# Kernel tuning notes

Measured on AMD Instinct MI355X. Metric: run time of the kernel, lower is better.

## Reference

```python
import jax, jax.numpy as jnp
import numpy as np

D_MODEL = 128; D_STATE = 16; D_CONV = 4; EXPAND = 2
D_INNER = EXPAND * D_MODEL          # 256
DT_RANK = (D_MODEL + 15) // 16      # 8 (ceil(d_model/16), Mamba default)
B, NF, H, W = 4, 32, 16, 16         # L = NF*H*W = 8192 tokens


def _layer_norm(x, w, b, eps=1e-5):
    m = x.mean(-1, keepdims=True)
    v = ((x - m) ** 2).mean(-1, keepdims=True)
    return (x - m) * jax.lax.rsqrt(v + eps) * w + b


def _causal_conv(x, w, b):
    # x: [B, L, D_INNER]; w: [D_INNER, 1, D_CONV] depthwise causal conv along L
    y = jax.lax.conv_general_dilated(
        jnp.swapaxes(x, 1, 2), w, (1,), [(D_CONV - 1, 0)],
        dimension_numbers=('NCH', 'OIH', 'NCH'), feature_group_count=D_INNER)
    return jnp.swapaxes(y + b[None, :, None], 1, 2)


def _mamba_dir(xi, z, conv_w, conv_b, xproj_w, dtproj_w, dtproj_b, A_log, Dskip):
    # One direction of the bidirectional Mamba block (selective scan).
    xc = jax.nn.silu(_causal_conv(xi, conv_w, conv_b))            # [B,L,Di]
    dbl = xc @ xproj_w.T                                          # [B,L,dt_rank+2n]
    dt_r, Bm, Cm = jnp.split(dbl, [DT_RANK, DT_RANK + D_STATE], axis=-1)
    dt = jax.nn.softplus(dt_r @ dtproj_w.T + dtproj_b)            # [B,L,Di]
    A = -jnp.exp(A_log)                                           # [Di,n]

    def step(h, inp):
        dt_t, B_t, C_t, x_t = inp                                 # [B,Di],[B,n],[B,n],[B,Di]
        h = jnp.exp(dt_t[:, :, None] * A) * h + (dt_t * x_t)[:, :, None] * B_t[:, None, :]
        return h, jnp.einsum('bdn,bn->bd', h, C_t)

    h0 = jnp.zeros((xi.shape[0], D_INNER, D_STATE), xi.dtype)
    xs = tuple(jnp.swapaxes(a, 0, 1) for a in (dt, Bm, Cm, xc))   # L-leading
    _, ys = jax.lax.scan(step, h0, xs)                            # [L,B,Di]
    y = jnp.swapaxes(ys, 0, 1) + xc * Dskip
    return y * jax.nn.silu(z)


def setup_inputs() -> dict:
    key = jax.random.key(0)
    ks = jax.random.split(key, 12)
    wrand = lambda k, shape: jax.random.normal(k, shape, jnp.float32) * 0.02
    # S4D-real init: A = [1..d_state] per channel
    A_init = jnp.log(jnp.tile(jnp.arange(1, D_STATE + 1, dtype=jnp.float32)[None, :], (D_INNER, 1)))
    dt_bias = jnp.full((D_INNER,), -4.6, jnp.float32)  # softplus^-1(~0.01)
    return {
        'x': jax.random.normal(ks[0], (B, D_MODEL, NF, H, W), jnp.float32),
        'ln1_w': jnp.ones((D_MODEL,), jnp.float32), 'ln1_b': jnp.zeros((D_MODEL,), jnp.float32),
        'ln2_w': jnp.ones((D_MODEL,), jnp.float32), 'ln2_b': jnp.zeros((D_MODEL,), jnp.float32),
        'in_proj_w': wrand(ks[1], (2 * D_INNER, D_MODEL)),
        'out_proj_w': wrand(ks[2], (D_MODEL, D_INNER)),
        'conv_w_f': wrand(ks[3], (D_INNER, 1, D_CONV)), 'conv_b_f': jnp.zeros((D_INNER,), jnp.float32),
        'xproj_w_f': wrand(ks[4], (DT_RANK + 2 * D_STATE, D_INNER)),
        'dtproj_w_f': wrand(ks[5], (D_INNER, DT_RANK)), 'dtproj_b_f': dt_bias,
        'A_log_f': A_init, 'D_f': jnp.ones((D_INNER,), jnp.float32),
        'conv_w_b': wrand(ks[6], (D_INNER, 1, D_CONV)), 'conv_b_b': jnp.zeros((D_INNER,), jnp.float32),
        'xproj_w_b': wrand(ks[7], (DT_RANK + 2 * D_STATE, D_INNER)),
        'dtproj_w_b': wrand(ks[8], (D_INNER, DT_RANK)), 'dtproj_b_b': dt_bias,
        'A_log_b': A_init, 'D_b': jnp.ones((D_INNER,), jnp.float32),
    }


def reference(x, ln1_w, ln1_b, ln2_w, ln2_b, in_proj_w, out_proj_w,
              conv_w_f, conv_b_f, xproj_w_f, dtproj_w_f, dtproj_b_f, A_log_f, D_f,
              conv_w_b, conv_b_b, xproj_w_b, dtproj_w_b, dtproj_b_b, A_log_b, D_b):
    b, d, nf, h, w = x.shape
    L = nf * h * w
    x_flat = jnp.swapaxes(x.reshape(b, d, L), 1, 2)               # [B,L,d_model]
    xn = _layer_norm(x_flat, ln1_w, ln1_b)
    xz = xn @ in_proj_w.T                                          # [B,L,2*Di]
    xi, z = jnp.split(xz, 2, axis=-1)
    y_f = _mamba_dir(xi, z, conv_w_f, conv_b_f, xproj_w_f, dtproj_w_f, dtproj_b_f, A_log_f, D_f)
    y_b = _mamba_dir(xi[:, ::-1], z[:, ::-1], conv_w_b, conv_b_b, xproj_w_b,
                     dtproj_w_b, dtproj_b_b, A_log_b, D_b)[:, ::-1]
    out = (y_f + y_b) @ out_proj_w.T                               # shared out_proj
    x_out = _layer_norm(x_flat + out, ln2_w, ln2_b)                # residual + norm2
    return jnp.swapaxes(x_out, 1, 2).reshape(b, d, nf, h, w)
```

## Files before the change

kernel.cpp:

```cpp
#include <hip/hip_runtime.h>

#define NB   4
#define LSEQ 8192
#define DM   128
#define DI   256
#define NS   16
#define RK   8
#define NCH  256
#define LC   32
#define MTOT (NB*LSEQ)
#define LOG2E 1.44269504088896340736f
#define LN2f  0.69314718055994530942f

#if __has_builtin(__builtin_amdgcn_exp2f)
__device__ __forceinline__ float fexp2(float x){ return __builtin_amdgcn_exp2f(x); }
#else
__device__ __forceinline__ float fexp2(float x){ return exp2f(x); }
#endif
#if __has_builtin(__builtin_amdgcn_logf)
__device__ __forceinline__ float flog2(float x){ return __builtin_amdgcn_logf(x); }
#else
__device__ __forceinline__ float flog2(float x){ return log2f(x); }
#endif
#if __has_builtin(__builtin_amdgcn_rcpf)
__device__ __forceinline__ float frcp(float x){ return __builtin_amdgcn_rcpf(x); }
#else
__device__ __forceinline__ float frcp(float x){ return 1.f/x; }
#endif
__device__ __forceinline__ float fexpn(float x){ return fexp2(x*LOG2E); }
__device__ __forceinline__ float fsilu(float x){ return x*frcp(1.f + fexpn(-x)); }
__device__ __forceinline__ float fsoftplus(float x){
  return fmaxf(x,0.f) + flog2(1.f + fexpn(-fabsf(x)))*LN2f;
}

__device__ __forceinline__ unsigned short f2bf(float v){
  unsigned int u = __float_as_uint(v);
  return (unsigned short)((u + 0x7FFFu + ((u >> 16) & 1u)) >> 16);
}
__device__ __forceinline__ float bf2f(unsigned short h){
  return __uint_as_float(((unsigned int)h) << 16);
}

typedef __attribute__((ext_vector_type(8))) short bf16x8;
typedef __attribute__((ext_vector_type(4))) float f32x4;
typedef __attribute__((ext_vector_type(2))) float f32x2;

#if __has_builtin(__builtin_elementwise_fma)
__device__ __forceinline__ f32x2 pkfma(f32x2 a, f32x2 b, f32x2 c){ return __builtin_elementwise_fma(a,b,c); }
#else
__device__ __forceinline__ f32x2 pkfma(f32x2 a, f32x2 b, f32x2 c){ return a*b + c; }
#endif

__global__ __launch_bounds__(256) void k_prep_w(
    const float* __restrict__ wip, unsigned short* __restrict__ wipbf,
    const float* __restrict__ xwf, const float* __restrict__ xwb, unsigned short* __restrict__ xwbf,
    const float* __restrict__ wop, unsigned short* __restrict__ wopbf)
{
  int i = blockIdx.x*256 + threadIdx.x;
  if (i < 65536) {
    wipbf[i] = f2bf(wip[i]);
  } else if (i < 90112) {
    int j = i - 65536;
    int dirw = j / 12288;
    int rem = j - dirw*12288;
    int row = rem >> 8, k = rem & 255;
    const float* src = dirw ? xwb : xwf;
    xwbf[j] = (row < 40) ? f2bf(src[row*256 + k]) : (unsigned short)0;
  } else {
    int j = i - 90112;
    wopbf[j] = f2bf(wop[j]);
  }
}

__global__ __launch_bounds__(256) void k_ln(
    const float* __restrict__ x, const float* __restrict__ ln1w, const float* __restrict__ ln1b,
    unsigned short* __restrict__ xnbf)
{
  __shared__ float a_s[DM][65];
  __shared__ float mS[64], rS[64];
  const int tid = threadIdx.x;
  const int m0 = blockIdx.x * 64;
  const int b = m0 >> 13, l0 = m0 & (LSEQ-1);
  const float* xb = x + b*DM*LSEQ;
#pragma unroll
  for (int i = 0; i < 32; ++i) {
    int idx = tid + i*256;
    int d = idx >> 6, l = idx & 63;
    a_s[d][l] = xb[d*LSEQ + l0 + l];
  }
  __syncthreads();
  {
    int p = tid & 3, l = tid >> 2;
    float s = 0.f, q = 0.f;
#pragma unroll
    for (int jj = 0; jj < 32; ++jj) {
      float v = a_s[p + 4*jj][l];
      s += v; q += v*v;
    }
    s += __shfl_xor(s,1); s += __shfl_xor(s,2);
    q += __shfl_xor(q,1); q += __shfl_xor(q,2);
    float m = s*(1.f/DM);
    float var = q*(1.f/DM) - m*m;
    if (p == 0) { mS[l] = m; rS[l] = rsqrtf(var + 1e-5f); }
  }
  __syncthreads();
#pragma unroll
  for (int i = 0; i < 32; ++i) {
    int idx = tid + i*256;
    int l = idx >> 7, d = idx & 127;
    float v = (a_s[d][l] - mS[l])*rS[l]*ln1w[d] + ln1b[d];
    xnbf[(m0+l)*DM + d] = f2bf(v);
  }
}

__global__ __launch_bounds__(256) void k_gemm_in(
    const unsigned short* __restrict__ xnbf, const unsigned short* __restrict__ wipbf,
    unsigned short* __restrict__ xib, unsigned short* __restrict__ zzb)
{
  __shared__ char lds[32768];
  const int tid = threadIdx.x;
  const int m0 = blockIdx.x * 64;
  const int n0 = blockIdx.y * 64;
  const unsigned short* srcs[2] = { xnbf + m0*DM, wipbf + n0*DM };
#pragma unroll
  for (int p = 0; p < 2; ++p) {
#pragma unroll
    for (int i = 0; i < 4; ++i) {
      int u = tid + i*256;
      int row = u >> 4, c = u & 15;
      int dstu = p*1024 + row*16 + (c ^ (row & 7));
      *(uint4*)(lds + dstu*16) = *(const uint4*)(srcs[p] + row*DM + c*8);
    }
  }
  __syncthreads();
  const int wid = tid >> 6, lane = tid & 63;
  const int m0w = (wid & 1)*32, n0w = (wid >> 1)*32;
  const int lr = lane & 15, kg = lane >> 4;
  bf16x8 af[2][4], bfv[2][4];
#pragma unroll
  for (int mi = 0; mi < 2; ++mi) {
    int row = m0w + mi*16 + lr;
#pragma unroll
    for (int kk = 0; kk < 4; ++kk) {
      int slot = (kk*4 + kg) ^ (row & 7);
      af[mi][kk] = *(const bf16x8*)(lds + row*256 + slot*16);
    }
  }
#pragma unroll
  for (int nj = 0; nj < 2; ++nj) {
    int row = n0w + nj*16 + lr;
#pragma unroll
    for (int kk = 0; kk < 4; ++kk) {
      int slot = (kk*4 + kg) ^ (row & 7);
      bfv[nj][kk] = *(const bf16x8*)(lds + 16384 + row*256 + slot*16);
    }
  }
  f32x4 acc[2][2];
#pragma unroll
  for (int mi = 0; mi < 2; ++mi)
#pragma unroll
    for (int nj = 0; nj < 2; ++nj) acc[mi][nj] = 0.f;
#pragma unroll
  for (int kk = 0; kk < 4; ++kk)
#pragma unroll
    for (int mi = 0; mi < 2; ++mi)
#pragma unroll
      for (int nj = 0; nj < 2; ++nj)
        acc[mi][nj] = __builtin_amdgcn_mfma_f32_16x16x32_bf16(af[mi][kk], bfv[nj][kk], acc[mi][nj], 0,0,0);
  if (n0 < 256) {
#pragma unroll
    for (int mi = 0; mi < 2; ++mi)
#pragma unroll
      for (int nj = 0; nj < 2; ++nj) {
        int n_g = n0 + n0w + nj*16 + lr;
#pragma unroll
        for (int r = 0; r < 4; ++r) {
          int m_g = m0 + m0w + mi*16 + kg*4 + r;
          xib[(size_t)m_g*DI + n_g] = f2bf(acc[mi][nj][r]);
        }
      }
  } else {
#pragma unroll
    for (int mi = 0; mi < 2; ++mi)
#pragma unroll
      for (int nj = 0; nj < 2; ++nj) {
        int n_g = (n0 - 256) + n0w + nj*16 + lr;
#pragma unroll
        for (int r = 0; r < 4; ++r) {
          int m_g = m0 + m0w + mi*16 + kg*4 + r;
          zzb[(size_t)m_g*DI + n_g] = f2bf(fsilu(acc[mi][nj][r]));
        }
      }
  }
}

__global__ __launch_bounds__(256) void k_conv_xproj(
  const unsigned short* __restrict__ xib,
  const float* __restrict__ cwf, const float* __restrict__ cbf,
  const float* __restrict__ cwb, const float* __restrict__ cbb,
  const unsigned short* __restrict__ xwbf,
  const float* __restrict__ dtwf, const float* __restrict__ dtbf,
  const float* __restrict__ dtwb, const float* __restrict__ dtbb,
  float* __restrict__ Bm, float* __restrict__ Cm,
  unsigned int* __restrict__ xdt)
{
  __shared__ char lds[57344];
  __shared__ float dtr_s[64][8];
  const int tid = threadIdx.x, bid = blockIdx.x;
  const int lt = bid & (LSEQ/64 - 1);
  const int b  = (bid >> 7) & 3;
  const int dir = bid >> 9;
  const int l0 = lt*64;
  const int db = dir*NB + b;
  const unsigned short* xwp = xwbf + dir*48*256;
#pragma unroll
  for (int i = 0; i < 6; ++i) {
    int u = tid + i*256;
    int row = u >> 5, s = u & 31;
    *(uint4*)(lds + 32768 + row*512 + ((s ^ (row & 7))<<4)) =
        *(const uint4*)(xwp + row*256 + s*8);
  }
  const float* cw  = dir ? cwb : cwf;
  const float* cbp = dir ? cbb : cbf;
  const int d = tid;
  const float w0 = cw[d*4+0], w1 = cw[d*4+1], w2 = cw[d*4+2], w3 = cw[d*4+3];
  const float bias = cbp[d];
  const int g0 = dir ? (LSEQ-1-l0) : l0;
  const int stp = dir ? -DI : DI;
  const unsigned short* xp = xib + (size_t)(b*LSEQ)*DI + d + (size_t)g0*DI;
  float h3 = 0.f, h2 = 0.f, h1 = 0.f;
  if (l0 >= 3) { h3 = bf2f(xp[-3*stp]); h2 = bf2f(xp[-2*stp]); h1 = bf2f(xp[-1*stp]); }
  float r0 = bf2f(xp[0]), r1 = bf2f(xp[stp]), r2 = bf2f(xp[2*stp]), r3 = bf2f(xp[3*stp]);
  for (int j = 0; j < 64; j += 4) {
    float v0 = r0, v1 = r1, v2 = r2, v3 = r3;
    if (j + 4 < 64) {
      const unsigned short* q = xp + (j+4)*stp;
      r0 = bf2f(q[0]); r1 = bf2f(q[stp]); r2 = bf2f(q[2*stp]); r3 = bf2f(q[3*stp]);
    }
#pragma unroll
    for (int u = 0; u < 4; ++u) {
      float vv = (u==0)?v0:(u==1)?v1:(u==2)?v2:v3;
      float a = bias + w0*h3 + w1*h2 + w2*h1 + w3*vv;
      int row = j + u;
      *(unsigned short*)(lds + row*512 + ((((d>>3) ^ (row&7))<<4) + ((d&7)<<1))) = f2bf(fsilu(a));
      h3 = h2; h2 = h1; h1 = vv;
    }
  }
  __syncthreads();
  const int wid = tid >> 6, lane = tid & 63;
  const int lr = lane & 15, kg = lane >> 4;
  const int arow = wid*16 + lr;
  f32x4 acc[3];
#pragma unroll
  for (int j = 0; j < 3; ++j) acc[j] = 0.f;
#pragma unroll
  for (int t = 0; t < 8; ++t) {
    bf16x8 afv = *(const bf16x8*)(lds + arow*512 + (((t*4+kg) ^ (arow&7))<<4));
#pragma unroll
    for (int j = 0; j < 3; ++j) {
      int wrow = j*16 + lr;
      bf16x8 bfr = *(const bf16x8*)(lds + 32768 + wrow*512 + (((t*4+kg) ^ (wrow&7))<<4));
      acc[j] = __builtin_amdgcn_mfma_f32_16x16x32_bf16(afv, bfr, acc[j], 0,0,0);
    }
  }
  const int base_l = (db*LSEQ + l0) + wid*16 + kg*4;
  const int rloc = wid*16 + kg*4;
#pragma unroll
  for (int j = 0; j < 3; ++j) {
    int col = j*16 + lr;
#pragma unroll
    for (int r = 0; r < 4; ++r) {
      float v = acc[j][r];
      if (col < 8)       dtr_s[rloc + r][col] = v;
      else if (col < 24) Bm[(size_t)(base_l + r)*NS + col - 8] = v;
      else if (col < 40) Cm[(size_t)(base_l + r)*NS + col - 24] = v;
    }
  }
  __syncthreads();
  const float* dtw = dir ? dtwb : dtwf;
  const float* dtbp= dir ? dtbb : dtbf;
  float dwv[8];
  *(float4*)(dwv+0) = *(const float4*)&dtw[d*RK];
  *(float4*)(dwv+4) = *(const float4*)&dtw[d*RK+4];
  const float dtbv = dtbp[d];
  unsigned int* xdtp = xdt + (size_t)(db*LSEQ + l0)*DI + d;
  for (int row = 0; row < 64; ++row) {
    float sd = dtbv;
#pragma unroll
    for (int r = 0; r < RK; ++r) sd = fmaf(dtr_s[row][r], dwv[r], sd);
    unsigned short dtb = f2bf(fsoftplus(sd));
    unsigned short xcb = *(const unsigned short*)(lds + row*512 + ((((d>>3) ^ (row&7))<<4) + ((d&7)<<1)));
    xdtp[(size_t)row*DI] = (unsigned int)xcb | ((unsigned int)dtb << 16);
  }
}

__global__ __launch_bounds__(256) void k_scan_local(
  const unsigned int* __restrict__ xdt, const float* __restrict__ Bm,
  const float* __restrict__ alogf, const float* __restrict__ alogb,
  unsigned short* __restrict__ hloc, float* __restrict__ sumdt)
{
  __shared__ float Bc[LC][NS];
  const int tid = threadIdx.x, bid = blockIdx.x;
  const int c = bid & (NCH-1), b = (bid>>8)&3, dir = bid>>10;
  const int db = dir*NB + b;
  const int l0 = c*LC;
  for (int i = tid; i < LC*NS; i += 256) (&Bc[0][0])[i] = Bm[(size_t)(db*LSEQ + l0)*NS + i];
  const float* alog = dir ? alogb : alogf;
  const int d = tid;
  float A2[NS];
#pragma unroll
  for (int n = 0; n < NS; ++n) A2[n] = -fexpn(alog[d*NS+n]) * LOG2E;
  const float a20 = A2[0];
  bool pw = true;
#pragma unroll
  for (int n = 1; n < NS; ++n) pw = pw && (fabsf(A2[n] - (n+1)*a20) <= 1e-3f*fabsf(A2[n]));
  f32x2 h2[8];
#pragma unroll
  for (int k = 0; k < 8; ++k) h2[k] = 0.f;
  const unsigned int* xp = xdt + (size_t)(db*LSEQ + l0)*DI + d;
  unsigned int u0 = xp[0], u1 = xp[DI], u2 = xp[2*DI], u3 = xp[3*DI];
  __syncthreads();
  float sac = 0.f;
  for (int j = 0; j < LC; j += 4) {
    unsigned int w0=u0, w1=u1, w2=u2, w3=u3;
    if (j + 4 < LC) {
      const unsigned int* q = xp + (size_t)(j+4)*DI;
      u0=q[0]; u1=q[DI]; u2=q[2*DI]; u3=q[3*DI];
    }
#pragma unroll
    for (int u = 0; u < 4; ++u) {
      unsigned int uu = (u==0)?w0:(u==1)?w1:(u==2)?w2:w3;
      float xc = __uint_as_float(uu << 16);
      float dt = __uint_as_float(uu & 0xffff0000u);
      sac += dt;
      float dx = dt*xc;
      f32x2 e2[8];
      if (pw) {
        float e1 = fexp2(a20*dt);
        float es = e1*e1;
        f32x2 esq = {es, es};
        e2[0] = (f32x2){e1, es};
#pragma unroll
        for (int k = 1; k < 8; ++k) e2[k] = e2[k-1]*esq;
      } else {
#pragma unroll
        for (int k = 0; k < 8; ++k)
          e2[k] = (f32x2){fexp2(A2[2*k]*dt), fexp2(A2[2*k+1]*dt)};
      }
      const f32x2* bb2 = (const f32x2*)&Bc[j+u][0];
      f32x2 dx2 = {dx, dx};
#pragma unroll
      for (int k = 0; k < 8; ++k) h2[k] = pkfma(h2[k], e2[k], bb2[k]*dx2);
    }
  }
  unsigned int hp8[8];
#pragma unroll
  for (int k = 0; k < 8; ++k)
    hp8[k] = (unsigned int)f2bf(h2[k].x) | ((unsigned int)f2bf(h2[k].y) << 16);
  unsigned short* dst = hloc + ((size_t)(db*NCH + c)*DI + d)*NS;
  *(uint4*)(dst)   = *(uint4*)(hp8);
  *(uint4*)(dst+8) = *(uint4*)(hp8+4);
  sumdt[(size_t)(db*NCH + c)*DI + d] = sac;
}

__global__ __launch_bounds__(64) void k_prefix(
  unsigned short* __restrict__ hloc, const float* __restrict__ sumdt,
  const float* __restrict__ alogf, const float* __restrict__ alogb)
{
  const int gid = blockIdx.x*64 + threadIdx.x;
  const int n = gid & 15;
  const int d = (gid >> 4) & 255;
  const int db = gid >> 12;
  const float* alog = (db >= NB) ? alogb : alogf;
  const float a2 = -fexpn(alog[d*NS+n]) * LOG2E;
  const int HS = DI*NS;
  unsigned short* hp = hloc + (size_t)db*NCH*HS + d*NS + n;
  const float* sp = sumdt + (size_t)db*NCH*DI + d;
  float hr = 0.f;
  float bl[16], bs[16];
#pragma unroll
  for (int j = 0; j < 16; ++j) { bl[j] = bf2f(hp[(size_t)j*HS]); bs[j] = sp[(size_t)j*DI]; }
  for (int blk = 0; blk < NCH/16; ++blk) {
    float nl[16], nsv[16];
    if (blk < NCH/16 - 1) {
#pragma unroll
      for (int j = 0; j < 16; ++j) {
        nl[j]  = bf2f(hp[(size_t)(blk*16+16+j)*HS]);
        nsv[j] = sp[(size_t)(blk*16+16+j)*DI];
      }
    }
#pragma unroll
    for (int j = 0; j < 16; ++j) {
      float hl = bl[j];
      hp[(size_t)(blk*16+j)*HS] = f2bf(hr);
      hr = fmaf(fexp2(a2*bs[j]), hr, hl);
    }
    if (blk < NCH/16 - 1) {
#pragma unroll
      for (int j = 0; j < 16; ++j) { bl[j] = nl[j]; bs[j] = nsv[j]; }
    }
  }
}

__global__ __launch_bounds__(256) void k_scan_out(
  const unsigned int* __restrict__ xdt, const unsigned short* __restrict__ zzb,
  const float* __restrict__ Bm, const float* __restrict__ Cm,
  const unsigned short* __restrict__ hinb,
  const float* __restrict__ alogf, const float* __restrict__ alogb,
  const float* __restrict__ Dskf, const float* __restrict__ Dskb,
  unsigned short* __restrict__ s2bf)
{
  __shared__ float Bc[LC][NS];
  __shared__ float Cc[LC][NS];
  const int tid = threadIdx.x, bid = blockIdx.x;
  const int c = bid & (NCH-1), b = (bid>>8)&3, dir = bid>>10;
  const int db = dir*NB + b;
  const int l0 = c*LC;
  for (int i = tid; i < LC*NS; i += 256) (&Bc[0][0])[i] = Bm[(size_t)(db*LSEQ + l0)*NS + i];
  for (int i = tid; i < LC*NS; i += 256) (&Cc[0][0])[i] = Cm[(size_t)(db*LSEQ + l0)*NS + i];
  const float* alog = dir ? alogb : alogf;
  const int d = tid;
  const float Dd = (dir ? Dskb : Dskf)[d];
  float A2[NS];
#pragma unroll
  for (int n = 0; n < NS; ++n) A2[n] = -fexpn(alog[d*NS+n]) * LOG2E;
  const float a20 = A2[0];
  bool pw = true;
#pragma unroll
  for (int n = 1; n < NS; ++n) pw = pw && (fabsf(A2[n] - (n+1)*a20) <= 1e-3f*fabsf(A2[n]));
  f32x2 h2[8];
  {
    const unsigned short* hb = hinb + ((size_t)(db*NCH + c)*DI + d)*NS;
    uint4 p0 = *(const uint4*)(hb);
    uint4 p1 = *(const uint4*)(hb+8);
    unsigned int w[8] = {p0.x,p0.y,p0.z,p0.w,p1.x,p1.y,p1.z,p1.w};
#pragma unroll
    for (int k = 0; k < 8; ++k)
      h2[k] = (f32x2){__uint_as_float(w[k] << 16), __uint_as_float(w[k] & 0xffff0000u)};
  }
  const int g0 = dir ? (LSEQ-1-l0) : l0;
  const int stp = dir ? -DI : DI;
  const unsigned int* xp = xdt + (size_t)(db*LSEQ + l0)*DI + d;
  const unsigned short* zp = zzb + (size_t)(b*LSEQ + g0)*DI + d;
  unsigned short* sp = s2bf + (size_t)(db*LSEQ + l0)*DI + d;
  unsigned int u0 = xp[0], u1 = xp[DI], u2 = xp[2*DI], u3 = xp[3*DI];
  unsigned short z0 = zp[0], z1 = zp[stp], z2 = zp[2*stp], z3 = zp[3*stp];
  __syncthreads();
  for (int j = 0; j < LC; j += 4) {
    unsigned int w0=u0, w1=u1, w2=u2, w3=u3;
    unsigned short y0=z0, y1=z1, y2=z2, y3=z3;
    if (j + 4 < LC) {
      const unsigned int* q = xp + (size_t)(j+4)*DI;
      u0=q[0]; u1=q[DI]; u2=q[2*DI]; u3=q[3*DI];
      const unsigned short* qz = zp + (j+4)*stp;
      z0=qz[0]; z1=qz[stp]; z2=qz[2*stp]; z3=qz[3*stp];
    }
#pragma unroll
    for (int u = 0; u < 4; ++u) {
      unsigned int uu = (u==0)?w0:(u==1)?w1:(u==2)?w2:w3;
      unsigned short zu = (u==0)?y0:(u==1)?y1:(u==2)?y2:y3;
      float xc = __uint_as_float(uu << 16);
      float dt = __uint_as_float(uu & 0xffff0000u);
      float dx = dt*xc;
      f32x2 e2[8];
      if (pw) {
        float e1 = fexp2(a20*dt);
        float es = e1*e1;
        f32x2 esq = {es, es};
        e2[0] = (f32x2){e1, es};
#pragma unroll
        for (int k = 1; k < 8; ++k) e2[k] = e2[k-1]*esq;
      } else {
#pragma unroll
        for (int k = 0; k < 8; ++k)
          e2[k] = (f32x2){fexp2(A2[2*k]*dt), fexp2(A2[2*k+1]*dt)};
      }
      const f32x2* bb2 = (const f32x2*)&Bc[j+u][0];
      const f32x2* cc2 = (const f32x2*)&Cc[j+u][0];
      f32x2 dx2 = {dx, dx};
      f32x2 yv2 = {0.f, 0.f};
#pragma unroll
      for (int k = 0; k < 8; ++k) {
        h2[k] = pkfma(h2[k], e2[k], bb2[k]*dx2);
        yv2 = pkfma(h2[k], cc2[k], yv2);
      }
      float yv = yv2.x + yv2.y;
      yv = fmaf(xc, Dd, yv);
      sp[(size_t)(j+u)*DI] = f2bf(yv * bf2f(zu));
    }
  }
}

__global__ __launch_bounds__(512) void k_out(
  const unsigned short* __restrict__ s2bf,
  const unsigned short* __restrict__ wopbf,
  const float* __restrict__ x, const float* __restrict__ ln2w, const float* __restrict__ ln2b,
  float* __restrict__ out)
{
  __shared__ char lds[65536];
  const int tid = threadIdx.x;
  const int m0 = blockIdx.x*64;
  const int b = m0 >> 13, l0 = m0 & (LSEQ-1);
  const unsigned short* sF = s2bf + (size_t)b*LSEQ*DI;
  const unsigned short* sB = s2bf + (size_t)(NB + b)*LSEQ*DI;
#pragma unroll
  for (int i = 0; i < 8; ++i) {
    int u = tid + i*512;
    int row = u >> 6, c = u & 63;
    int l = l0 + row;
    const unsigned short* src = (c < 32) ? (sF + (size_t)l*DI + c*8)
                                         : (sB + (size_t)(LSEQ-1-l)*DI + (c-32)*8);
    *(uint4*)(lds + row*1024 + ((c ^ (row & 7))<<4)) = *(const uint4*)src;
  }
  const int wid = tid >> 6;
  const int wr = wid >> 2, wc = wid & 3;
  const int lane = tid & 63, lr = lane & 15, kg = lane >> 4;
  bf16x8 wf[2][8];
#pragma unroll
  for (int nt = 0; nt < 2; ++nt) {
    int n = wc*32 + nt*16 + lr;
#pragma unroll
    for (int kt = 0; kt < 8; ++kt)
      wf[nt][kt] = *(const bf16x8*)(wopbf + n*DI + kt*32 + kg*8);
  }
  __syncthreads();
  f32x4 acc[2][2];
#pragma unroll
  for (int mt = 0; mt < 2; ++mt)
#pragma unroll
    for (int nt = 0; nt < 2; ++nt) acc[mt][nt] = 0.f;
#pragma unroll
  for (int kt2 = 0; kt2 < 16; ++kt2) {
#pragma unroll
    for (int mt = 0; mt < 2; ++mt) {
      int row = wr*32 + mt*16 + lr;
      int slot = (kt2*4 + kg) ^ (row & 7);
      bf16x8 af = *(const bf16x8*)(lds + row*1024 + (slot<<4));
#pragma unroll
      for (int nt = 0; nt < 2; ++nt)
        acc[mt][nt] = __builtin_amdgcn_mfma_f32_16x16x32_bf16(af, wf[nt][kt2 & 7], acc[mt][nt], 0,0,0);
    }
  }
  __syncthreads();
  float* smem = (float*)lds;
  const int RP = 133;
  float* mS = smem + 64*RP;
  float* rS = mS + 64;
  const float* xb = x + b*DM*LSEQ + l0;
#pragma unroll
  for (int mt = 0; mt < 2; ++mt) {
    int mbase = wr*32 + mt*16 + kg*4;
#pragma unroll
    for (int nt = 0; nt < 2; ++nt) {
      int n = wc*32 + nt*16 + lr;
      float4 rx = *(const float4*)&xb[n*LSEQ + mbase];
      smem[(mbase+0)*RP + n] = acc[mt][nt][0] + rx.x;
      smem[(mbase+1)*RP + n] = acc[mt][nt][1] + rx.y;
      smem[(mbase+2)*RP + n] = acc[mt][nt][2] + rx.z;
      smem[(mbase+3)*RP + n] = acc[mt][nt][3] + rx.w;
    }
  }
  __syncthreads();
  {
    int row = tid >> 3, p = tid & 7;
    float s = 0.f, q = 0.f;
#pragma unroll
    for (int jj = 0; jj < 16; ++jj) {
      float v = smem[row*RP + p*16 + jj];
      s += v; q += v*v;
    }
    s += __shfl_xor(s,1); s += __shfl_xor(s,2); s += __shfl_xor(s,4);
    q += __shfl_xor(q,1); q += __shfl_xor(q,2); q += __shfl_xor(q,4);
    if (p == 0) {
      float m = s*(1.f/DM);
      float var = q*(1.f/DM) - m*m;
      mS[row] = m; rS[row] = rsqrtf(var + 1e-5f);
    }
  }
  __syncthreads();
  float* ob = out + b*DM*LSEQ + l0;
#pragma unroll
  for (int i = 0; i < 16; ++i) {
    int idx = tid + i*512;
    int col = idx >> 6, l = idx & 63;
    float v = (smem[l*RP + col] - mS[l])*rS[l]*ln2w[col] + ln2b[col];
    ob[col*LSEQ + l] = v;
  }
}

extern "C" void kernel_launch(void* const* d_in, const int* in_sizes, int n_in,
                              void* d_out, int out_size, void* d_ws, size_t ws_size,
                              hipStream_t stream)
{
  (void)in_sizes; (void)n_in; (void)out_size; (void)ws_size;
  const float* x     = (const float*)d_in[0];
  const float* ln1w  = (const float*)d_in[1];
  const float* ln1b  = (const float*)d_in[2];
  const float* ln2w  = (const float*)d_in[3];
  const float* ln2b  = (const float*)d_in[4];
  const float* wip   = (const float*)d_in[5];
  const float* wop   = (const float*)d_in[6];
  const float* cwf   = (const float*)d_in[7];
  const float* cbf   = (const float*)d_in[8];
  const float* xwf   = (const float*)d_in[9];
  const float* dtwf  = (const float*)d_in[10];
  const float* dtbf  = (const float*)d_in[11];
  const float* alogf = (const float*)d_in[12];
  const float* Dskf  = (const float*)d_in[13];
  const float* cwb   = (const float*)d_in[14];
  const float* cbb   = (const float*)d_in[15];
  const float* xwb   = (const float*)d_in[16];
  const float* dtwb  = (const float*)d_in[17];
  const float* dtbb  = (const float*)d_in[18];
  const float* alogb = (const float*)d_in[19];
  const float* Dskb  = (const float*)d_in[20];

  float* ws    = (float*)d_ws;
  float* xibF  = ws;
  float* zzbF  = xibF  + 4194304;
  float* Bm    = zzbF  + 4194304;
  float* Cm    = Bm    + 1048576;
  float* s2F   = Cm    + 1048576;
  float* xdtF  = s2F   + 8388608;
  float* hlocF = xdtF  + 16777216;
  float* sumdt = hlocF + 4194304;
  float* xwbfF = sumdt + 524288;
  float* wopbfF= xwbfF + 12288;
  float* out   = (float*)d_out;
  unsigned short* xnbf  = (unsigned short*)s2F;
  unsigned short* wipbf = (unsigned short*)(s2F + 2097152);
  unsigned short* s2bf  = (unsigned short*)s2F;
  unsigned short* xib   = (unsigned short*)xibF;
  unsigned short* zzb   = (unsigned short*)zzbF;
  unsigned int*   xdt   = (unsigned int*)xdtF;
  unsigned short* hloc  = (unsigned short*)hlocF;
  unsigned short* xwbf  = (unsigned short*)xwbfF;
  unsigned short* wopbf = (unsigned short*)wopbfF;

  k_prep_w<<<480, 256, 0, stream>>>(wip, wipbf, xwf, xwb, xwbf, wop, wopbf);
  k_ln<<<512, 256, 0, stream>>>(x, ln1w, ln1b, xnbf);
  k_gemm_in<<<dim3(512,8), 256, 0, stream>>>(xnbf, wipbf, xib, zzb);
  k_conv_xproj<<<1024, 256, 0, stream>>>(xib, cwf,cbf,cwb,cbb, xwbf,
                                         dtwf,dtbf,dtwb,dtbb, Bm, Cm, xdt);
  k_scan_local<<<2048, 256, 0, stream>>>(xdt, Bm, alogf, alogb, hloc, sumdt);
  k_prefix<<<512, 64, 0, stream>>>(hloc, sumdt, alogf, alogb);
  k_scan_out<<<2048, 256, 0, stream>>>(xdt, zzb, Bm, Cm, hloc,
                                       alogf, alogb, Dskf, Dskb, s2bf);
  k_out<<<512, 512, 0, stream>>>(s2bf, wopbf, x, ln2w, ln2b, out);
}
```

Baseline: 153.7 us.

## Loop in_proj GEMM over all N tiles per block to reuse A tile

The input-projection GEMM now launches one block per 64-row M tile instead of a 512x8 grid. Each block stages the A tile in LDS once and loops over the eight 64-column N tiles. B fragments are read directly from global memory (the small weight should stay cached) instead of being staged in LDS. This removes the eightfold reload of the activation tile and halves LDS use, at the cost of fewer blocks and a serial loop per block.

```diff
diff --git a/kernel.cpp b/kernel.cpp
--- a/kernel.cpp
+++ b/kernel.cpp
@@ -117,26 +117,22 @@
     const unsigned short* __restrict__ xnbf, const unsigned short* __restrict__ wipbf,
     unsigned short* __restrict__ xib, unsigned short* __restrict__ zzb)
 {
-  __shared__ char lds[32768];
+  __shared__ char lds[16384];
   const int tid = threadIdx.x;
   const int m0 = blockIdx.x * 64;
-  const int n0 = blockIdx.y * 64;
-  const unsigned short* srcs[2] = { xnbf + m0*DM, wipbf + n0*DM };
-#pragma unroll
-  for (int p = 0; p < 2; ++p) {
-#pragma unroll
-    for (int i = 0; i < 4; ++i) {
-      int u = tid + i*256;
-      int row = u >> 4, c = u & 15;
-      int dstu = p*1024 + row*16 + (c ^ (row & 7));
-      *(uint4*)(lds + dstu*16) = *(const uint4*)(srcs[p] + row*DM + c*8);
-    }
+  const unsigned short* asrc = xnbf + (size_t)m0*DM;
+#pragma unroll
+  for (int i = 0; i < 4; ++i) {
+    int u = tid + i*256;
+    int row = u >> 4, c = u & 15;
+    int dstu = row*16 + (c ^ (row & 7));
+    *(uint4*)(lds + dstu*16) = *(const uint4*)(asrc + row*DM + c*8);
   }
   __syncthreads();
   const int wid = tid >> 6, lane = tid & 63;
-  const int m0w = (wid & 1)*32, n0w = (wid >> 1)*32;
+  const int m0w = (wid & 1)*32, nql = (wid >> 1)*32;
   const int lr = lane & 15, kg = lane >> 4;
-  bf16x8 af[2][4], bfv[2][4];
+  bf16x8 af[2][4];
 #pragma unroll
   for (int mi = 0; mi < 2; ++mi) {
     int row = m0w + mi*16 + lr;
@@ -146,51 +142,53 @@
       af[mi][kk] = *(const bf16x8*)(lds + row*256 + slot*16);
     }
   }
-#pragma unroll
-  for (int nj = 0; nj < 2; ++nj) {
-    int row = n0w + nj*16 + lr;
-#pragma unroll
-    for (int kk = 0; kk < 4; ++kk) {
-      int slot = (kk*4 + kg) ^ (row & 7);
-      bfv[nj][kk] = *(const bf16x8*)(lds + 16384 + row*256 + slot*16);
-    }
-  }
-  f32x4 acc[2][2];
-#pragma unroll
-  for (int mi = 0; mi < 2; ++mi)
-#pragma unroll
-    for (int nj = 0; nj < 2; ++nj) acc[mi][nj] = 0.f;
-#pragma unroll
-  for (int kk = 0; kk < 4; ++kk)
+  for (int t = 0; t < 8; ++t) {
+    const int n0 = t*64;
+    bf16x8 bfv[2][4];
+#pragma unroll
+    for (int nj = 0; nj < 2; ++nj) {
+      int nrow = n0 + nql + nj*16 + lr;
+#pragma unroll
+      for (int kk = 0; kk < 4; ++kk)
+        bfv[nj][kk] = *(const bf16x8*)(wipbf + nrow*DM + kk*32 + kg*8);
+    }
+    f32x4 acc[2][2];
 #pragma unroll
     for (int mi = 0; mi < 2; ++mi)
 #pragma unroll
-      for (int nj = 0; nj < 2; ++nj)
-        acc[mi][nj] = __builtin_amdgcn_mfma_f32_16x16x32_bf16(af[mi][kk], bfv[nj][kk], acc[mi][nj], 0,0,0);
-  if (n0 < 256) {
-#pragma unroll
-    for (int mi = 0; mi < 2; ++mi)
-#pragma unroll
-      for (int nj = 0; nj < 2; ++nj) {
-        int n_g = n0 + n0w + nj*16 + lr;
-#pragma unroll
-        for (int r = 0; r < 4; ++r) {
-          int m_g = m0 + m0w + mi*16 + kg*4 + r;
-          xib[(size_t)m_g*DI + n_g] = f2bf(acc[mi][nj][r]);
+      for (int nj = 0; nj < 2; ++nj) acc[mi][nj] = 0.f;
+#pragma unroll
+    for (int kk = 0; kk < 4; ++kk)
+#pragma unroll
+      for (int mi = 0; mi < 2; ++mi)
+#pragma unroll
+        for (int nj = 0; nj < 2; ++nj)
+          acc[mi][nj] = __builtin_amdgcn_mfma_f32_16x16x32_bf16(af[mi][kk], bfv[nj][kk], acc[mi][nj], 0,0,0);
+    if (t < 4) {
+#pragma unroll
+      for (int mi = 0; mi < 2; ++mi)
+#pragma unroll
+        for (int nj = 0; nj < 2; ++nj) {
+          int n_g = n0 + nql + nj*16 + lr;
+#pragma unroll
+          for (int r = 0; r < 4; ++r) {
+            int m_g = m0 + m0w + mi*16 + kg*4 + r;
+            xib[(size_t)m_g*DI + n_g] = f2bf(acc[mi][nj][r]);
+          }
         }
-      }
-  } else {
-#pragma unroll
-    for (int mi = 0; mi < 2; ++mi)
-#pragma unroll
-      for (int nj = 0; nj < 2; ++nj) {
-        int n_g = (n0 - 256) + n0w + nj*16 + lr;
-#pragma unroll
-        for (int r = 0; r < 4; ++r) {
-          int m_g = m0 + m0w + mi*16 + kg*4 + r;
-          zzb[(size_t)m_g*DI + n_g] = f2bf(fsilu(acc[mi][nj][r]));
+    } else {
+#pragma unroll
+      for (int mi = 0; mi < 2; ++mi)
+#pragma unroll
+        for (int nj = 0; nj < 2; ++nj) {
+          int n_g = (n0 - 256) + nql + nj*16 + lr;
+#pragma unroll
+          for (int r = 0; r < 4; ++r) {
+            int m_g = m0 + m0w + mi*16 + kg*4 + r;
+            zzb[(size_t)m_g*DI + n_g] = f2bf(fsilu(acc[mi][nj][r]));
+          }
         }
-      }
+    }
   }
 }
 
@@ -639,7 +637,7 @@
 
   k_prep_w<<<480, 256, 0, stream>>>(wip, wipbf, xwf, xwb, xwbf, wop, wopbf);
   k_ln<<<512, 256, 0, stream>>>(x, ln1w, ln1b, xnbf);
-  k_gemm_in<<<dim3(512,8), 256, 0, stream>>>(xnbf, wipbf, xib, zzb);
+  k_gemm_in<<<512, 256, 0, stream>>>(xnbf, wipbf, xib, zzb);
   k_conv_xproj<<<1024, 256, 0, stream>>>(xib, cwf,cbf,cwb,cbb, xwbf,
                                          dtwf,dtbf,dtwb,dtbb, Bm, Cm, xdt);
   k_scan_local<<<2048, 256, 0, stream>>>(xdt, Bm, alogf, alogb, hloc, sumdt);
```

New measurement: 162.7 us. +5.9%, slower.
